# Kernel optimization log

Hardware: AMD Instinct MI355X
Metric: run time of the kernel (lower is better)

The kernel has to match this reference:

```python
import jax, jax.numpy as jnp
import numpy as np

NEG = -10000.0
EPS = 1e-5

B, N, H, DEPTH = 4096, 64, 128, 3
H2 = H // 2


def setup_inputs() -> dict:
    key = jax.random.key(0)
    k1, k2, k3 = jax.random.split(key, 3)
    hidden_states = jax.random.normal(k1, (B, N, H), dtype=jnp.float32)
    li_vector_num = jax.random.randint(k2, (B,), 0, N + 1, dtype=jnp.int32)
    Ws = jax.random.normal(k3, (DEPTH, H, H2), dtype=jnp.float32) * (1.0 / np.sqrt(H))
    bs = jnp.zeros((DEPTH, H2), dtype=jnp.float32)
    ln_w = jnp.ones((DEPTH, H2), dtype=jnp.float32)
    ln_b = jnp.zeros((DEPTH, H2), dtype=jnp.float32)
    return {"hidden_states": hidden_states, "li_vector_num": li_vector_num,
            "Ws": Ws, "bs": bs, "ln_w": ln_w, "ln_b": ln_b}


def _subgraph(hidden_states, Ws, bs, ln_w, ln_b, li_vector_num):
    b, n, h = hidden_states.shape
    # padding mask: -10000 for invalid vectors (i >= li_vector_num), per polyline
    pad = jnp.where(jnp.arange(n)[None, :] >= li_vector_num[:, None], NEG, 0.0)
    pad = pad.astype(hidden_states.dtype)[:, :, None]  # [B,N,1]
    hs = hidden_states
    for l in range(Ws.shape[0]):
        # MLP: linear -> layernorm -> relu
        x = jnp.einsum('bnh,hk->bnk', hs, Ws[l]) + bs[l]
        mu = jnp.mean(x, axis=-1, keepdims=True)
        var = jnp.mean((x - mu) ** 2, axis=-1, keepdims=True)
        x = ln_w[l] * (x - mu) * jax.lax.rsqrt(var + EPS) + ln_b[l]
        enc = jax.nn.relu(x)  # [B,N,H2]
        m = enc + pad  # masked encoded states
        # leave-one-out max over vector dim via top-2 trick (replaces O(N^2) loop)
        top2 = jax.lax.top_k(jnp.swapaxes(m, 1, 2), 2)[0]  # [B,H2,2]
        top1b = top2[..., 0][:, None, :]  # [B,1,H2]
        top2b = top2[..., 1][:, None, :]  # [B,1,H2]
        loo = jnp.where(m == top1b, top2b, top1b)  # max over i != j
        loo = jnp.maximum(loo, m + NEG)            # faithful: j itself at -10000
        loo = jnp.maximum(loo, 0.0)                # torch.max(max_hidden, zeros)
        hs = jnp.concatenate([enc, loo], axis=-1)  # [B,N,H]
    return jnp.max(hs, axis=1)  # [B,H]


def reference(hidden_states, li_vector_num, Ws, bs, ln_w, ln_b):
    return _subgraph(hidden_states, Ws, bs, ln_w, ln_b, li_vector_num)
```

## Files before the change

### kernel.cpp

```cpp
#include <hip/hip_runtime.h>
#include <hip/hip_bf16.h>

#define NEGV (-10000.0f)
#define EPSV (1e-5f)
#define NINF (-3.4e38f)

typedef __attribute__((ext_vector_type(8))) short short8;
typedef __attribute__((ext_vector_type(4))) float floatx4;

constexpr int Bsz = 4096, Nv = 64, Hd = 128, DEPTH = 3, H2 = 64;
constexpr int ESTR = 72;

struct alignas(8) BH4 { __hip_bfloat162 a, b; };

__device__ __forceinline__ unsigned short f2b(float f) {
    unsigned int u = __builtin_bit_cast(unsigned int, f);
    u += 0x7fffu + ((u >> 16) & 1u);
    return (unsigned short)(u >> 16);
}

template <int CTRL>
__device__ __forceinline__ float dpp_add(float v) {
    int y = __builtin_amdgcn_update_dpp(0, __builtin_bit_cast(int, v), CTRL, 0xf, 0xf, true);
    return v + __builtin_bit_cast(float, y);
}
__device__ __forceinline__ float sum16(float v) {
    v = dpp_add<0xB1>(v);
    v = dpp_add<0x4E>(v);
    v = dpp_add<0x124>(v);
    v = dpp_add<0x128>(v);
    return v;
}

__device__ __forceinline__ void t2insIdx(float& t1, float& t2, unsigned& i1,
                                         float v, unsigned iv) {
    bool c = v > t1;
    float lo = fminf(t1, v);
    t1 = fmaxf(t1, v);
    i1 = c ? iv : i1;
    t2 = fmaxf(t2, lo);
}

__global__ void prep_w(const float* __restrict__ Ws, unsigned short* __restrict__ wt) {
    int idx = blockIdx.x * 256 + threadIdx.x;
    if (idx < DEPTH * 8192) {
        int l = idx >> 13, o = idx & 8191;
        int j = o & 7, q = (o >> 3) & 63, hi = (o >> 9) & 3, kt = o >> 11;
        int k = kt * 32 + hi * 8 + j;
        int srccol = (q & 15) * 4 + (q >> 4);
        wt[idx] = f2b(Ws[l * 8192 + k * 64 + srccol]);
    }
}

__global__ __launch_bounds__(256, 3)
void subgraph_kernel(const float* __restrict__ hidden, const int* __restrict__ lvn,
                     const unsigned short* __restrict__ wt,
                     const float* __restrict__ bsv, const float* __restrict__ lnw,
                     const float* __restrict__ lnb, float* __restrict__ out)
{
    __shared__ __hip_bfloat16 encs[2][4][16][ESTR];
    __shared__ float fbuf3[4][4][2][3][64];
    __shared__ float apk[2][64][2];
    __shared__ unsigned short aidx[2][64];

    const int t = threadIdx.x;
    const int lane = t & 63, wid = t >> 6;
    const int b0 = blockIdx.x * 2;
    const int lr = lane & 15, hi = lane >> 4;
    const int L0 = lvn[b0], L1 = lvn[b0 + 1];
    const unsigned myrow = wid * 16 + lr;

    float madd[2][4];
#pragma unroll
    for (int p = 0; p < 2; ++p)
#pragma unroll
        for (int reg = 0; reg < 4; ++reg)
            madd[p][reg] = ((int)(wid * 16 + hi * 4 + reg) >= (p ? L1 : L0)) ? NEGV : 0.0f;

    const float4* ab0 = (const float4*)(hidden + (size_t)b0 * Nv * Hd);
    const float4* ab1 = ab0 + (Nv * Hd) / 4;

#pragma unroll
    for (int l = 0; l < DEPTH; ++l) {
        const short8* wfrag = (const short8*)(wt + l * 8192);

        short8 af[2][4];
        if (l == 0) {
#pragma unroll
            for (int p = 0; p < 2; ++p) {
                const float4* ab = p ? ab1 : ab0;
#pragma unroll
                for (int kt = 0; kt < 4; ++kt) {
                    int fi = (int)myrow * 32 + kt * 8 + hi * 2;
                    float4 f0 = ab[fi], f1 = ab[fi + 1];
                    union { short8 s; __hip_bfloat162 h[4]; } u;
                    u.h[0] = __float22bfloat162_rn(make_float2(f0.x, f0.y));
                    u.h[1] = __float22bfloat162_rn(make_float2(f0.z, f0.w));
                    u.h[2] = __float22bfloat162_rn(make_float2(f1.x, f1.y));
                    u.h[3] = __float22bfloat162_rn(make_float2(f1.z, f1.w));
                    af[p][kt] = u.s;
                }
            }
        } else {
#pragma unroll
            for (int p = 0; p < 2; ++p) {
                af[p][0] = *(const short8*)&encs[p][wid][lr][hi * 8];
                af[p][1] = *(const short8*)&encs[p][wid][lr][32 + hi * 8];
            }
#pragma unroll
            for (int kt = 2; kt < 4; ++kt) {
                int cbase = (kt - 2) * 32 + hi * 8;
#pragma unroll
                for (int p = 0; p < 2; ++p) {
                    short8 ar = *(const short8*)&aidx[p][cbase];
                    const float4* ap = (const float4*)&apk[p][0][0];
                    int fb = cbase >> 1;
                    float4 q0 = ap[fb], q1 = ap[fb + 1], q2 = ap[fb + 2], q3 = ap[fb + 3];
                    unsigned pk1s[8] = {
                        __builtin_bit_cast(unsigned, q0.x), __builtin_bit_cast(unsigned, q0.z),
                        __builtin_bit_cast(unsigned, q1.x), __builtin_bit_cast(unsigned, q1.z),
                        __builtin_bit_cast(unsigned, q2.x), __builtin_bit_cast(unsigned, q2.z),
                        __builtin_bit_cast(unsigned, q3.x), __builtin_bit_cast(unsigned, q3.z)};
                    unsigned pk2s[8] = {
                        __builtin_bit_cast(unsigned, q0.y), __builtin_bit_cast(unsigned, q0.w),
                        __builtin_bit_cast(unsigned, q1.y), __builtin_bit_cast(unsigned, q1.w),
                        __builtin_bit_cast(unsigned, q2.y), __builtin_bit_cast(unsigned, q2.w),
                        __builtin_bit_cast(unsigned, q3.y), __builtin_bit_cast(unsigned, q3.w)};
                    union { short8 s; unsigned u[4]; } uu;
#pragma unroll
                    for (int j2 = 0; j2 < 4; ++j2) {
                        unsigned s0 = ((unsigned)(unsigned short)ar[2 * j2]     == myrow)
                                      ? pk2s[2 * j2]     : pk1s[2 * j2];
                        unsigned s1 = ((unsigned)(unsigned short)ar[2 * j2 + 1] == myrow)
                                      ? pk2s[2 * j2 + 1] : pk1s[2 * j2 + 1];
                        uu.u[j2] = __builtin_amdgcn_perm(s1, s0, 0x05040100u);
                    }
                    af[p][kt] = uu.s;
                }
            }
        }

        floatx4 acc[2][4];
#pragma unroll
        for (int p = 0; p < 2; ++p)
#pragma unroll
            for (int ct = 0; ct < 4; ++ct) { floatx4 z = {0.f, 0.f, 0.f, 0.f}; acc[p][ct] = z; }
#pragma unroll
        for (int kt = 0; kt < 4; ++kt)
#pragma unroll
            for (int ct = 0; ct < 4; ++ct) {
                short8 bf = wfrag[(kt * 4 + hi) * 64 + ct * 16 + lr];
                acc[0][ct] = __builtin_amdgcn_mfma_f32_16x16x32_bf16(af[0][kt], bf, acc[0][ct], 0, 0, 0);
                acc[1][ct] = __builtin_amdgcn_mfma_f32_16x16x32_bf16(af[1][kt], bf, acc[1][ct], 0, 0, 0);
            }

        float4 bias = *(const float4*)(bsv + l * H2 + 4 * lr);
        float4 gwv  = *(const float4*)(lnw + l * H2 + 4 * lr);
        float4 gbv  = *(const float4*)(lnb + l * H2 + 4 * lr);
#pragma unroll
        for (int p = 0; p < 2; ++p)
#pragma unroll
            for (int reg = 0; reg < 4; ++reg) {
                float x0 = acc[p][0][reg] + bias.x;
                float x1 = acc[p][1][reg] + bias.y;
                float x2 = acc[p][2][reg] + bias.z;
                float x3 = acc[p][3][reg] + bias.w;
                float s = sum16((x0 + x1) + (x2 + x3));
                float q = sum16((x0 * x0 + x1 * x1) + (x2 * x2 + x3 * x3));
                float mu  = s * (1.0f / 64.0f);
                float var = fmaxf(q * (1.0f / 64.0f) - mu * mu, 0.0f);
                float rstd = rsqrtf(var + EPSV);
                acc[p][0][reg] = fmaxf(gwv.x * (x0 - mu) * rstd + gbv.x, 0.0f);
                acc[p][1][reg] = fmaxf(gwv.y * (x1 - mu) * rstd + gbv.y, 0.0f);
                acc[p][2][reg] = fmaxf(gwv.z * (x2 - mu) * rstd + gbv.z, 0.0f);
                acc[p][3][reg] = fmaxf(gwv.w * (x3 - mu) * rstd + gbv.w, 0.0f);
            }

        if (l < DEPTH - 1) {
#pragma unroll
            for (int p = 0; p < 2; ++p) {
                float t1v[4] = {NINF, NINF, NINF, NINF}, t2v[4] = {NINF, NINF, NINF, NINF};
                unsigned i1v[4] = {0, 0, 0, 0};
#pragma unroll
                for (int reg = 0; reg < 4; ++reg) {
                    BH4 we;
                    we.a = __float22bfloat162_rn(make_float2(acc[p][0][reg], acc[p][1][reg]));
                    we.b = __float22bfloat162_rn(make_float2(acc[p][2][reg], acc[p][3][reg]));
                    *(BH4*)&encs[p][wid][hi * 4 + reg][4 * lr] = we;
                    float mk = madd[p][reg];
                    unsigned rowi = wid * 16 + hi * 4 + reg;
                    t2insIdx(t1v[0], t2v[0], i1v[0], acc[p][0][reg] + mk, rowi);
                    t2insIdx(t1v[1], t2v[1], i1v[1], acc[p][1][reg] + mk, rowi);
                    t2insIdx(t1v[2], t2v[2], i1v[2], acc[p][2][reg] + mk, rowi);
                    t2insIdx(t1v[3], t2v[3], i1v[3], acc[p][3][reg] + mk, rowi);
                }
                *(float4*)&fbuf3[wid][hi][p][0][4 * lr] = make_float4(t1v[0], t1v[1], t1v[2], t1v[3]);
                *(float4*)&fbuf3[wid][hi][p][1][4 * lr] = make_float4(t2v[0], t2v[1], t2v[2], t2v[3]);
                *(float4*)&fbuf3[wid][hi][p][2][4 * lr] = make_float4(
                    __builtin_bit_cast(float, i1v[0]), __builtin_bit_cast(float, i1v[1]),
                    __builtin_bit_cast(float, i1v[2]), __builtin_bit_cast(float, i1v[3]));
            }
            __syncthreads();

            if (t < 128) {
                int p = t >> 6, c = t & 63;
                float m1 = NINF, m2 = NINF; unsigned a1 = 0;
#pragma unroll
                for (int w = 0; w < 4; ++w)
#pragma unroll
                    for (int h = 0; h < 4; ++h) {
                        float o1 = fbuf3[w][h][p][0][c], o2 = fbuf3[w][h][p][1][c];
                        unsigned io = __builtin_bit_cast(unsigned, fbuf3[w][h][p][2][c]);
                        bool cg = o1 > m1;
                        float lo = fminf(m1, o1);
                        m1 = fmaxf(m1, o1);
                        a1 = cg ? io : a1;
                        m2 = fmaxf(fmaxf(m2, o2), lo);
                    }
                float F1 = fmaxf(m1, 0.0f), F2 = fmaxf(m2, 0.0f);
                apk[p][c][0] = __builtin_bit_cast(float, (unsigned)f2b(F1));
                apk[p][c][1] = __builtin_bit_cast(float, (unsigned)f2b(F2));
                aidx[p][c] = (unsigned short)a1;
            }
            __syncthreads();
        } else {
#pragma unroll
            for (int p = 0; p < 2; ++p) {
                float t1v[4], em4[4];
#pragma unroll
                for (int ct = 0; ct < 4; ++ct) {
                    float a = acc[p][ct][0], b = acc[p][ct][1];
                    float c2 = acc[p][ct][2], d = acc[p][ct][3];
                    em4[ct] = fmaxf(fmaxf(a, b), fmaxf(c2, d));
                    t1v[ct] = fmaxf(fmaxf(a + madd[p][0], b + madd[p][1]),
                                    fmaxf(c2 + madd[p][2], d + madd[p][3]));
                }
                *(float4*)&fbuf3[wid][hi][p][0][4 * lr] = make_float4(t1v[0], t1v[1], t1v[2], t1v[3]);
                *(float4*)&fbuf3[wid][hi][p][1][4 * lr] = make_float4(em4[0], em4[1], em4[2], em4[3]);
            }
            __syncthreads();

            if (t < 128) {
                int p = t >> 6, c = t & 63;
                float mm = NINF, me = NINF;
#pragma unroll
                for (int w = 0; w < 4; ++w)
#pragma unroll
                    for (int h = 0; h < 4; ++h) {
                        mm = fmaxf(mm, fbuf3[w][h][p][0][c]);
                        me = fmaxf(me, fbuf3[w][h][p][1][c]);
                    }
                out[(size_t)(b0 + p) * Hd + c]      = me;
                out[(size_t)(b0 + p) * Hd + 64 + c] = fmaxf(mm, 0.0f);
            }
        }
    }
}

extern "C" void kernel_launch(void* const* d_in, const int* in_sizes, int n_in,
                              void* d_out, int out_size, void* d_ws, size_t ws_size,
                              hipStream_t stream) {
    const float* hidden = (const float*)d_in[0];
    const int*   lvn    = (const int*)d_in[1];
    const float* Ws     = (const float*)d_in[2];
    const float* bs     = (const float*)d_in[3];
    const float* lnwp   = (const float*)d_in[4];
    const float* lnbp   = (const float*)d_in[5];
    unsigned short* wt  = (unsigned short*)d_ws;
    float* outp = (float*)d_out;

    prep_w<<<(DEPTH * 8192 + 255) / 256, 256, 0, stream>>>(Ws, wt);
    subgraph_kernel<<<Bsz / 2, 256, 0, stream>>>(hidden, lvn, wt, bs, lnwp, lnbp, outp);
}
```

Before: 56.21 us.

## Overlap enc-half MFMAs with top-2 reduction and pack argmax index into value bits

Restructures the layer loop so the MFMAs over the enc half of the next layer's input (columns 0-63) run right after writing encs, while threads 0-127 perform the cross-wave top-2 reduction, before the second barrier. It also packs the argmax row index into the low 6 mantissa bits of the top-1 value, cutting the shared-memory reduction buffer from three slots to two and dropping one LDS store and load per element. The weight fragments for the loo half are loaded ahead of the gather. The bit-packing perturbs top-1 values slightly and can alter tie-breaking, which is a small accuracy risk.

```diff
diff --git a/kernel.cpp b/kernel.cpp
--- a/kernel.cpp
+++ b/kernel.cpp
@@ -59,7 +59,7 @@
                      const float* __restrict__ lnb, float* __restrict__ out)
 {
     __shared__ __hip_bfloat16 encs[2][4][16][ESTR];
-    __shared__ float fbuf3[4][4][2][3][64];
+    __shared__ float fb[4][4][2][2][64];
     __shared__ float apk[2][64][2];
     __shared__ unsigned short aidx[2][64];
 
@@ -80,71 +80,30 @@
     const float4* ab0 = (const float4*)(hidden + (size_t)b0 * Nv * Hd);
     const float4* ab1 = ab0 + (Nv * Hd) / 4;
 
-#pragma unroll
-    for (int l = 0; l < DEPTH; ++l) {
-        const short8* wfrag = (const short8*)(wt + l * 8192);
-
+    floatx4 acc[2][4];
+
+    {
+        const short8* wfrag = (const short8*)wt;
         short8 af[2][4];
-        if (l == 0) {
-#pragma unroll
-            for (int p = 0; p < 2; ++p) {
-                const float4* ab = p ? ab1 : ab0;
-#pragma unroll
-                for (int kt = 0; kt < 4; ++kt) {
-                    int fi = (int)myrow * 32 + kt * 8 + hi * 2;
-                    float4 f0 = ab[fi], f1 = ab[fi + 1];
-                    union { short8 s; __hip_bfloat162 h[4]; } u;
-                    u.h[0] = __float22bfloat162_rn(make_float2(f0.x, f0.y));
-                    u.h[1] = __float22bfloat162_rn(make_float2(f0.z, f0.w));
-                    u.h[2] = __float22bfloat162_rn(make_float2(f1.x, f1.y));
-                    u.h[3] = __float22bfloat162_rn(make_float2(f1.z, f1.w));
-                    af[p][kt] = u.s;
-                }
-            }
-        } else {
-#pragma unroll
-            for (int p = 0; p < 2; ++p) {
-                af[p][0] = *(const short8*)&encs[p][wid][lr][hi * 8];
-                af[p][1] = *(const short8*)&encs[p][wid][lr][32 + hi * 8];
-            }
-#pragma unroll
-            for (int kt = 2; kt < 4; ++kt) {
-                int cbase = (kt - 2) * 32 + hi * 8;
-#pragma unroll
-                for (int p = 0; p < 2; ++p) {
-                    short8 ar = *(const short8*)&aidx[p][cbase];
-                    const float4* ap = (const float4*)&apk[p][0][0];
-                    int fb = cbase >> 1;
-                    float4 q0 = ap[fb], q1 = ap[fb + 1], q2 = ap[fb + 2], q3 = ap[fb + 3];
-                    unsigned pk1s[8] = {
-                        __builtin_bit_cast(unsigned, q0.x), __builtin_bit_cast(unsigned, q0.z),
-                        __builtin_bit_cast(unsigned, q1.x), __builtin_bit_cast(unsigned, q1.z),
-                        __builtin_bit_cast(unsigned, q2.x), __builtin_bit_cast(unsigned, q2.z),
-                        __builtin_bit_cast(unsigned, q3.x), __builtin_bit_cast(unsigned, q3.z)};
-                    unsigned pk2s[8] = {
-                        __builtin_bit_cast(unsigned, q0.y), __builtin_bit_cast(unsigned, q0.w),
-                        __builtin_bit_cast(unsigned, q1.y), __builtin_bit_cast(unsigned, q1.w),
-                        __builtin_bit_cast(unsigned, q2.y), __builtin_bit_cast(unsigned, q2.w),
-                        __builtin_bit_cast(unsigned, q3.y), __builtin_bit_cast(unsigned, q3.w)};
-                    union { short8 s; unsigned u[4]; } uu;
-#pragma unroll
-                    for (int j2 = 0; j2 < 4; ++j2) {
-                        unsigned s0 = ((unsigned)(unsigned short)ar[2 * j2]     == myrow)
-                                      ? pk2s[2 * j2]     : pk1s[2 * j2];
-                        unsigned s1 = ((unsigned)(unsigned short)ar[2 * j2 + 1] == myrow)
-                                      ? pk2s[2 * j2 + 1] : pk1s[2 * j2 + 1];
-                        uu.u[j2] = __builtin_amdgcn_perm(s1, s0, 0x05040100u);
-                    }
-                    af[p][kt] = uu.s;
-                }
-            }
-        }
-
-        floatx4 acc[2][4];
+#pragma unroll
+        for (int p = 0; p < 2; ++p) {
+            const float4* ab = p ? ab1 : ab0;
+#pragma unroll
+            for (int kt = 0; kt < 4; ++kt) {
+                int fi = (int)myrow * 32 + kt * 8 + hi * 2;
+                float4 f0 = ab[fi], f1 = ab[fi + 1];
+                union { short8 s; __hip_bfloat162 h[4]; } u;
+                u.h[0] = __float22bfloat162_rn(make_float2(f0.x, f0.y));
+                u.h[1] = __float22bfloat162_rn(make_float2(f0.z, f0.w));
+                u.h[2] = __float22bfloat162_rn(make_float2(f1.x, f1.y));
+                u.h[3] = __float22bfloat162_rn(make_float2(f1.z, f1.w));
+                af[p][kt] = u.s;
+            }
+        }
 #pragma unroll
         for (int p = 0; p < 2; ++p)
 #pragma unroll
-            for (int ct = 0; ct < 4; ++ct) { floatx4 z = {0.f, 0.f, 0.f, 0.f}; acc[p][ct] = z; }
+            for (int ct = 0; ct < 4; ++ct) { floatx4 z = {0.f,0.f,0.f,0.f}; acc[p][ct] = z; }
 #pragma unroll
         for (int kt = 0; kt < 4; ++kt)
 #pragma unroll
@@ -153,10 +112,9 @@
                 acc[0][ct] = __builtin_amdgcn_mfma_f32_16x16x32_bf16(af[0][kt], bf, acc[0][ct], 0, 0, 0);
                 acc[1][ct] = __builtin_amdgcn_mfma_f32_16x16x32_bf16(af[1][kt], bf, acc[1][ct], 0, 0, 0);
             }
-
-        float4 bias = *(const float4*)(bsv + l * H2 + 4 * lr);
-        float4 gwv  = *(const float4*)(lnw + l * H2 + 4 * lr);
-        float4 gbv  = *(const float4*)(lnb + l * H2 + 4 * lr);
+        float4 bias = *(const float4*)(bsv + 4 * lr);
+        float4 gwv  = *(const float4*)(lnw + 4 * lr);
+        float4 gbv  = *(const float4*)(lnb + 4 * lr);
 #pragma unroll
         for (int p = 0; p < 2; ++p)
 #pragma unroll
@@ -175,85 +133,170 @@
                 acc[p][2][reg] = fmaxf(gwv.z * (x2 - mu) * rstd + gbv.z, 0.0f);
                 acc[p][3][reg] = fmaxf(gwv.w * (x3 - mu) * rstd + gbv.w, 0.0f);
             }
-
-        if (l < DEPTH - 1) {
+    }
+
+#pragma unroll
+    for (int lt = 0; lt < 2; ++lt) {
+        const short8* wnx = (const short8*)(wt + (lt + 1) * 8192);
+
+#pragma unroll
+        for (int p = 0; p < 2; ++p) {
+            float t1v[4] = {NINF, NINF, NINF, NINF}, t2v[4] = {NINF, NINF, NINF, NINF};
+            unsigned i1v[4] = {0, 0, 0, 0};
+#pragma unroll
+            for (int reg = 0; reg < 4; ++reg) {
+                BH4 we;
+                we.a = __float22bfloat162_rn(make_float2(acc[p][0][reg], acc[p][1][reg]));
+                we.b = __float22bfloat162_rn(make_float2(acc[p][2][reg], acc[p][3][reg]));
+                *(BH4*)&encs[p][wid][hi * 4 + reg][4 * lr] = we;
+                float mk = madd[p][reg];
+                unsigned rowi = wid * 16 + hi * 4 + reg;
+                t2insIdx(t1v[0], t2v[0], i1v[0], acc[p][0][reg] + mk, rowi);
+                t2insIdx(t1v[1], t2v[1], i1v[1], acc[p][1][reg] + mk, rowi);
+                t2insIdx(t1v[2], t2v[2], i1v[2], acc[p][2][reg] + mk, rowi);
+                t2insIdx(t1v[3], t2v[3], i1v[3], acc[p][3][reg] + mk, rowi);
+            }
+            float4 w0, w1;
+#pragma unroll
+            for (int ct = 0; ct < 4; ++ct) {
+                unsigned bits = (__builtin_bit_cast(unsigned, t1v[ct]) & ~63u) | i1v[ct];
+                (&w0.x)[ct] = __builtin_bit_cast(float, bits);
+                (&w1.x)[ct] = t2v[ct];
+            }
+            *(float4*)&fb[wid][hi][p][0][4 * lr] = w0;
+            *(float4*)&fb[wid][hi][p][1][4 * lr] = w1;
+        }
+        __syncthreads();
+
+        if (t < 128) {
+            int p = t >> 6, c = t & 63;
+            float m1 = NINF, m2 = NINF; unsigned a1 = 0;
+#pragma unroll
+            for (int w = 0; w < 4; ++w)
+#pragma unroll
+                for (int h = 0; h < 4; ++h) {
+                    float o1 = fb[w][h][p][0][c], o2 = fb[w][h][p][1][c];
+                    bool cg = o1 > m1;
+                    float lo = fminf(m1, o1);
+                    m1 = fmaxf(m1, o1);
+                    a1 = cg ? (__builtin_bit_cast(unsigned, o1) & 63u) : a1;
+                    m2 = fmaxf(fmaxf(m2, o2), lo);
+                }
+            apk[p][c][0] = __builtin_bit_cast(float, (unsigned)f2b(fmaxf(m1, 0.0f)));
+            apk[p][c][1] = __builtin_bit_cast(float, (unsigned)f2b(fmaxf(m2, 0.0f)));
+            aidx[p][c] = (unsigned short)a1;
+        }
+
+        short8 af01[2][2];
+#pragma unroll
+        for (int p = 0; p < 2; ++p) {
+            af01[p][0] = *(const short8*)&encs[p][wid][lr][hi * 8];
+            af01[p][1] = *(const short8*)&encs[p][wid][lr][32 + hi * 8];
+        }
+#pragma unroll
+        for (int p = 0; p < 2; ++p)
+#pragma unroll
+            for (int ct = 0; ct < 4; ++ct) { floatx4 z = {0.f,0.f,0.f,0.f}; acc[p][ct] = z; }
+#pragma unroll
+        for (int kt = 0; kt < 2; ++kt)
+#pragma unroll
+            for (int ct = 0; ct < 4; ++ct) {
+                short8 bf = wnx[(kt * 4 + hi) * 64 + ct * 16 + lr];
+                acc[0][ct] = __builtin_amdgcn_mfma_f32_16x16x32_bf16(af01[0][kt], bf, acc[0][ct], 0, 0, 0);
+                acc[1][ct] = __builtin_amdgcn_mfma_f32_16x16x32_bf16(af01[1][kt], bf, acc[1][ct], 0, 0, 0);
+            }
+        __syncthreads();
+
+#pragma unroll
+        for (int kt = 2; kt < 4; ++kt) {
+            int cbase = (kt - 2) * 32 + hi * 8;
+            short8 bfr[4];
+#pragma unroll
+            for (int ct = 0; ct < 4; ++ct)
+                bfr[ct] = wnx[(kt * 4 + hi) * 64 + ct * 16 + lr];
 #pragma unroll
             for (int p = 0; p < 2; ++p) {
-                float t1v[4] = {NINF, NINF, NINF, NINF}, t2v[4] = {NINF, NINF, NINF, NINF};
-                unsigned i1v[4] = {0, 0, 0, 0};
-#pragma unroll
-                for (int reg = 0; reg < 4; ++reg) {
-                    BH4 we;
-                    we.a = __float22bfloat162_rn(make_float2(acc[p][0][reg], acc[p][1][reg]));
-                    we.b = __float22bfloat162_rn(make_float2(acc[p][2][reg], acc[p][3][reg]));
-                    *(BH4*)&encs[p][wid][hi * 4 + reg][4 * lr] = we;
-                    float mk = madd[p][reg];
-                    unsigned rowi = wid * 16 + hi * 4 + reg;
-                    t2insIdx(t1v[0], t2v[0], i1v[0], acc[p][0][reg] + mk, rowi);
-                    t2insIdx(t1v[1], t2v[1], i1v[1], acc[p][1][reg] + mk, rowi);
-                    t2insIdx(t1v[2], t2v[2], i1v[2], acc[p][2][reg] + mk, rowi);
-                    t2insIdx(t1v[3], t2v[3], i1v[3], acc[p][3][reg] + mk, rowi);
+                short8 ar = *(const short8*)&aidx[p][cbase];
+                const float4* ap = (const float4*)&apk[p][0][0];
+                int fbq = cbase >> 1;
+                float4 q0 = ap[fbq], q1 = ap[fbq + 1], q2 = ap[fbq + 2], q3 = ap[fbq + 3];
+                unsigned pk1s[8] = {
+                    __builtin_bit_cast(unsigned, q0.x), __builtin_bit_cast(unsigned, q0.z),
+                    __builtin_bit_cast(unsigned, q1.x), __builtin_bit_cast(unsigned, q1.z),
+                    __builtin_bit_cast(unsigned, q2.x), __builtin_bit_cast(unsigned, q2.z),
+                    __builtin_bit_cast(unsigned, q3.x), __builtin_bit_cast(unsigned, q3.z)};
+                unsigned pk2s[8] = {
+                    __builtin_bit_cast(unsigned, q0.y), __builtin_bit_cast(unsigned, q0.w),
+                    __builtin_bit_cast(unsigned, q1.y), __builtin_bit_cast(unsigned, q1.w),
+                    __builtin_bit_cast(unsigned, q2.y), __builtin_bit_cast(unsigned, q2.w),
+                    __builtin_bit_cast(unsigned, q3.y), __builtin_bit_cast(unsigned, q3.w)};
+                union { short8 s; unsigned u[4]; } uu;
+#pragma unroll
+                for (int j2 = 0; j2 < 4; ++j2) {
+                    unsigned s0 = ((unsigned)(unsigned short)ar[2 * j2]     == myrow)
+                                  ? pk2s[2 * j2]     : pk1s[2 * j2];
+                    unsigned s1 = ((unsigned)(unsigned short)ar[2 * j2 + 1] == myrow)
+                                  ? pk2s[2 * j2 + 1] : pk1s[2 * j2 + 1];
+                    uu.u[j2] = __builtin_amdgcn_perm(s1, s0, 0x05040100u);
                 }
-                *(float4*)&fbuf3[wid][hi][p][0][4 * lr] = make_float4(t1v[0], t1v[1], t1v[2], t1v[3]);
-                *(float4*)&fbuf3[wid][hi][p][1][4 * lr] = make_float4(t2v[0], t2v[1], t2v[2], t2v[3]);
-                *(float4*)&fbuf3[wid][hi][p][2][4 * lr] = make_float4(
-                    __builtin_bit_cast(float, i1v[0]), __builtin_bit_cast(float, i1v[1]),
-                    __builtin_bit_cast(float, i1v[2]), __builtin_bit_cast(float, i1v[3]));
-            }
-            __syncthreads();
-
-            if (t < 128) {
-                int p = t >> 6, c = t & 63;
-                float m1 = NINF, m2 = NINF; unsigned a1 = 0;
-#pragma unroll
-                for (int w = 0; w < 4; ++w)
-#pragma unroll
-                    for (int h = 0; h < 4; ++h) {
-                        float o1 = fbuf3[w][h][p][0][c], o2 = fbuf3[w][h][p][1][c];
-                        unsigned io = __builtin_bit_cast(unsigned, fbuf3[w][h][p][2][c]);
-                        bool cg = o1 > m1;
-                        float lo = fminf(m1, o1);
-                        m1 = fmaxf(m1, o1);
-                        a1 = cg ? io : a1;
-                        m2 = fmaxf(fmaxf(m2, o2), lo);
-                    }
-                float F1 = fmaxf(m1, 0.0f), F2 = fmaxf(m2, 0.0f);
-                apk[p][c][0] = __builtin_bit_cast(float, (unsigned)f2b(F1));
-                apk[p][c][1] = __builtin_bit_cast(float, (unsigned)f2b(F2));
-                aidx[p][c] = (unsigned short)a1;
-            }
-            __syncthreads();
-        } else {
-#pragma unroll
-            for (int p = 0; p < 2; ++p) {
-                float t1v[4], em4[4];
-#pragma unroll
-                for (int ct = 0; ct < 4; ++ct) {
-                    float a = acc[p][ct][0], b = acc[p][ct][1];
-                    float c2 = acc[p][ct][2], d = acc[p][ct][3];
-                    em4[ct] = fmaxf(fmaxf(a, b), fmaxf(c2, d));
-                    t1v[ct] = fmaxf(fmaxf(a + madd[p][0], b + madd[p][1]),
-                                    fmaxf(c2 + madd[p][2], d + madd[p][3]));
-                }
-                *(float4*)&fbuf3[wid][hi][p][0][4 * lr] = make_float4(t1v[0], t1v[1], t1v[2], t1v[3]);
-                *(float4*)&fbuf3[wid][hi][p][1][4 * lr] = make_float4(em4[0], em4[1], em4[2], em4[3]);
-            }
-            __syncthreads();
-
-            if (t < 128) {
-                int p = t >> 6, c = t & 63;
-                float mm = NINF, me = NINF;
-#pragma unroll
-                for (int w = 0; w < 4; ++w)
-#pragma unroll
-                    for (int h = 0; h < 4; ++h) {
-                        mm = fmaxf(mm, fbuf3[w][h][p][0][c]);
-                        me = fmaxf(me, fbuf3[w][h][p][1][c]);
-                    }
-                out[(size_t)(b0 + p) * Hd + c]      = me;
-                out[(size_t)(b0 + p) * Hd + 64 + c] = fmaxf(mm, 0.0f);
-            }
-        }
+#pragma unroll
+                for (int ct = 0; ct < 4; ++ct)
+                    acc[p][ct] = __builtin_amdgcn_mfma_f32_16x16x32_bf16(uu.s, bfr[ct], acc[p][ct], 0, 0, 0);
+            }
+        }
+
+        float4 bias = *(const float4*)(bsv + (lt + 1) * H2 + 4 * lr);
+        float4 gwv  = *(const float4*)(lnw + (lt + 1) * H2 + 4 * lr);
+        float4 gbv  = *(const float4*)(lnb + (lt + 1) * H2 + 4 * lr);
+#pragma unroll
+        for (int p = 0; p < 2; ++p)
+#pragma unroll
+            for (int reg = 0; reg < 4; ++reg) {
+                float x0 = acc[p][0][reg] + bias.x;
+                float x1 = acc[p][1][reg] + bias.y;
+                float x2 = acc[p][2][reg] + bias.z;
+                float x3 = acc[p][3][reg] + bias.w;
+                float s = sum16((x0 + x1) + (x2 + x3));
+                float q = sum16((x0 * x0 + x1 * x1) + (x2 * x2 + x3 * x3));
+                float mu  = s * (1.0f / 64.0f);
+                float var = fmaxf(q * (1.0f / 64.0f) - mu * mu, 0.0f);
+                float rstd = rsqrtf(var + EPSV);
+                acc[p][0][reg] = fmaxf(gwv.x * (x0 - mu) * rstd + gbv.x, 0.0f);
+                acc[p][1][reg] = fmaxf(gwv.y * (x1 - mu) * rstd + gbv.y, 0.0f);
+                acc[p][2][reg] = fmaxf(gwv.z * (x2 - mu) * rstd + gbv.z, 0.0f);
+                acc[p][3][reg] = fmaxf(gwv.w * (x3 - mu) * rstd + gbv.w, 0.0f);
+            }
+        __syncthreads();
+    }
+
+#pragma unroll
+    for (int p = 0; p < 2; ++p) {
+        float t1v[4], em4[4];
+#pragma unroll
+        for (int ct = 0; ct < 4; ++ct) {
+            float a = acc[p][ct][0], b2 = acc[p][ct][1];
+            float c2 = acc[p][ct][2], d = acc[p][ct][3];
+            em4[ct] = fmaxf(fmaxf(a, b2), fmaxf(c2, d));
+            t1v[ct] = fmaxf(fmaxf(a + madd[p][0], b2 + madd[p][1]),
+                            fmaxf(c2 + madd[p][2], d + madd[p][3]));
+        }
+        *(float4*)&fb[wid][hi][p][0][4 * lr] = make_float4(t1v[0], t1v[1], t1v[2], t1v[3]);
+        *(float4*)&fb[wid][hi][p][1][4 * lr] = make_float4(em4[0], em4[1], em4[2], em4[3]);
+    }
+    __syncthreads();
+
+    if (t < 128) {
+        int p = t >> 6, c = t & 63;
+        float mm = NINF, me = NINF;
+#pragma unroll
+        for (int w = 0; w < 4; ++w)
+#pragma unroll
+            for (int h = 0; h < 4; ++h) {
+                mm = fmaxf(mm, fb[w][h][p][0][c]);
+                me = fmaxf(me, fb[w][h][p][1][c]);
+            }
+        out[(size_t)(b0 + p) * Hd + c]      = me;
+        out[(size_t)(b0 + p) * Hd + 64 + c] = fmaxf(mm, 0.0f);
     }
 }
 
```

Result: no change. 56.82 us (+1.1%).
